# Optimization experiments

Measured on AMD Instinct MI355X. Metric: run time of the kernel, lower is better.

Reference implementation:

```python
import jax, jax.numpy as jnp
import numpy as np

EMBED_DIM = 512
NUM_HEADS = 8
HEAD_DIM = EMBED_DIM // NUM_HEADS


def setup_inputs() -> dict:
    key = jax.random.key(0)
    ks = jax.random.split(key, 6)
    B, S, E = 2, 4096, EMBED_DIM
    scale = 1.0 / np.sqrt(E)
    return {
        "rotation_params": jax.random.normal(ks[0], (E, E), jnp.float32) * scale,
        "entangle_params": jax.random.normal(ks[1], (E, E), jnp.float32) * scale,
        "inputs": jax.random.normal(ks[2], (B, S, E), jnp.float32),
        "w_q": jax.random.normal(ks[3], (E, E), jnp.float32) * scale,
        "w_k": jax.random.normal(ks[4], (E, E), jnp.float32) * scale,
        "w_v": jax.random.normal(ks[5], (E, E), jnp.float32) * scale,
    }


def reference(rotation_params, entangle_params, inputs, w_q, w_k, w_v):
    B, S, E = inputs.shape
    H, D = NUM_HEADS, HEAD_DIM
    # torch nn.Linear(x) = x @ W.T ; then extra matmul with rotation/entangle mats
    q = (inputs @ w_q.T) @ rotation_params  # [B,S,E]
    k = (inputs @ w_k.T) @ entangle_params  # [B,S,E]
    v = inputs @ w_v.T                       # [B,S,E]
    # split heads -> [B,H,S,D]
    q = q.reshape(B, S, H, D).transpose(0, 2, 1, 3)
    k = k.reshape(B, S, H, D).transpose(0, 2, 1, 3)
    v = v.reshape(B, S, H, D).transpose(0, 2, 1, 3)
    scores = jnp.einsum("bhqd,bhkd->bhqk", q, k) / jnp.sqrt(jnp.float32(D))
    attn = jax.nn.softmax(scores, axis=-1)  # dropout p=0 (eval) -> identity
    out = jnp.einsum("bhqk,bhkd->bhqd", attn, v)
    return out.transpose(0, 2, 1, 3).reshape(B, S, E)
```

## Files before the change

### kernel.cpp

```cpp
#include <hip/hip_runtime.h>
#include <cstddef>

#define E 512
#define H 8
#define D 64
#define BATCH 2
#define SEQ 4096

typedef __attribute__((ext_vector_type(8))) short bf16x8;
typedef __attribute__((ext_vector_type(4))) float f32x4;
typedef __attribute__((ext_vector_type(16))) float f32x16;
typedef __attribute__((ext_vector_type(4))) unsigned uint4v;

__device__ __forceinline__ ushort f2bf(float f) {
  unsigned u = __builtin_bit_cast(unsigned, f);
  u += 0x7fff + ((u >> 16) & 1);
  return (ushort)(u >> 16);
}
__device__ __forceinline__ float bf2f(ushort h) {
  return __builtin_bit_cast(float, (unsigned)h << 16);
}
__device__ __forceinline__ unsigned pk_bf16(float lo, float hi) {
#if __has_builtin(__builtin_amdgcn_cvt_pk_bf16_f32)
  typedef __attribute__((ext_vector_type(2))) __bf16 bfv2;
  bfv2 r = __builtin_amdgcn_cvt_pk_bf16_f32(lo, hi);
  return __builtin_bit_cast(unsigned, r);
#else
  return (unsigned)f2bf(lo) | ((unsigned)f2bf(hi) << 16);
#endif
}
__device__ __forceinline__ float fexp2(float x) {
#if __has_builtin(__builtin_amdgcn_exp2f)
  return __builtin_amdgcn_exp2f(x);
#else
  return exp2f(x);
#endif
}
__device__ __forceinline__ void permswap32(unsigned& a, unsigned& b) {
  asm("v_permlane32_swap_b32 %0, %1" : "+v"(a), "+v"(b));
}

__global__ __launch_bounds__(256) void xcast(const float* __restrict__ x,
                                             ushort* __restrict__ xh,
                                             ushort* __restrict__ xl) {
  size_t i = ((size_t)blockIdx.x * 256 + threadIdx.x) * 4;
  float4 v = *(const float4*)&x[i];
  ushort4 h, l;
  h.x = f2bf(v.x); l.x = f2bf(v.x - bf2f(h.x));
  h.y = f2bf(v.y); l.y = f2bf(v.y - bf2f(h.y));
  h.z = f2bf(v.z); l.z = f2bf(v.z - bf2f(h.z));
  h.w = f2bf(v.w); l.w = f2bf(v.w - bf2f(h.w));
  *(ushort4*)&xh[i] = h;
  *(ushort4*)&xl[i] = l;
}

__global__ __launch_bounds__(256) void fold_tiled(
    const float* __restrict__ wq, const float* __restrict__ wk,
    const float* __restrict__ rot, const float* __restrict__ ent,
    ushort* __restrict__ weffbT) {
  const int which = blockIdx.z;
  const float* w = which ? wk : wq;
  const float* r = which ? ent : rot;
  const int k = blockIdx.x * 256 + threadIdx.x;
  const int n0 = blockIdx.y * 8;
  float acc[8] = {};
  for (int j0 = 0; j0 < E; j0 += 16) {
    float wv_[16];
#pragma unroll
    for (int u = 0; u < 16; ++u) wv_[u] = w[(size_t)(j0 + u) * E + k];
#pragma unroll
    for (int u = 0; u < 16; ++u)
#pragma unroll
      for (int t = 0; t < 8; ++t)
        acc[t] += wv_[u] * r[(size_t)(j0 + u) * E + n0 + t];
  }
#pragma unroll
  for (int t = 0; t < 8; ++t)
    weffbT[(size_t)which * E * E + (size_t)(n0 + t) * E + k] = f2bf(acc[t]);
}

__global__ __launch_bounds__(256) void wv_cast(const float* __restrict__ wv,
                                               ushort* __restrict__ dst) {
  size_t i = ((size_t)blockIdx.x * 256 + threadIdx.x) * 4;
  float4 v = *(const float4*)&wv[i];
  ushort4 o;
  o.x = f2bf(v.x); o.y = f2bf(v.y); o.z = f2bf(v.z); o.w = f2bf(v.w);
  *(ushort4*)&dst[i] = o;
}

#define LDQ 72
#define LDS_S 136

__global__ __launch_bounds__(512, 4) void qkv_fused(
    const ushort* __restrict__ xhg, const ushort* __restrict__ xlg,
    const ushort* __restrict__ weffbT, ushort* __restrict__ qg,
    ushort* __restrict__ kg, ushort* __restrict__ vtg) {
  __shared__ ushort sm[(128 + 128 + 192) * LDQ];
  ushort* Ah = sm;
  ushort* Al = sm + 128 * LDQ;
  ushort* Bs = sm + 256 * LDQ;
  ushort* vt_lds = Bs;

  const int lin = blockIdx.y * 8 + blockIdx.x;
  const int nl = (lin & 7) * 64 + (lin >> 3);
  const int head = nl & 7;
  const int m0 = (nl >> 3) * 128;

  const int tid = threadIdx.x;
  const int wave = tid >> 6, lane = tid & 63;
  const int l31 = lane & 31, hi = lane >> 5;
  const int wm = wave & 3, wn = wave >> 2;

  const int ar = tid >> 2, ac8 = (tid & 3) * 8;
  const int b1r = tid >> 2;
  const int b2r = 128 + ((tid >> 2) & 63);

  const ushort* arow = xhg + (size_t)(m0 + ar) * E + ac8;
  const ushort* lrow = xlg + (size_t)(m0 + ar) * E + ac8;
  const ushort* b1row =
      weffbT + (size_t)(b1r >> 6) * E * E + (size_t)(head * 64 + (b1r & 63)) * E + ac8;
  const ushort* b2row =
      weffbT + (size_t)2 * E * E + (size_t)(head * 64 + (b2r & 63)) * E + ac8;

  f32x16 acc[3];
  acc[0] = 0.f;
  acc[1] = 0.f;
  acc[2] = 0.f;

  uint4 pa_h = *(const uint4*)&arow[0];
  uint4 pa_l = *(const uint4*)&lrow[0];
  uint4 pb1 = *(const uint4*)&b1row[0];
  uint4 pb2 = (tid < 256) ? *(const uint4*)&b2row[0] : uint4{0, 0, 0, 0};

  const ushort* Ar = Ah + (wm * 32 + l31) * LDQ;
  const ushort* Lr = Al + (wm * 32 + l31) * LDQ;
  const ushort* Br = Bs + (wn * 96 + l31) * LDQ;

  for (int k0 = 0; k0 < E; k0 += 32) {
    __syncthreads();
    *(uint4*)&Ah[ar * LDQ + ac8] = pa_h;
    *(uint4*)&Al[ar * LDQ + ac8] = pa_l;
    *(uint4*)&Bs[b1r * LDQ + ac8] = pb1;
    if (tid < 256) *(uint4*)&Bs[b2r * LDQ + ac8] = pb2;
    __syncthreads();

    const int kn = (k0 + 32 < E) ? k0 + 32 : 0;
    pa_h = *(const uint4*)&arow[kn];
    pa_l = *(const uint4*)&lrow[kn];
    pb1 = *(const uint4*)&b1row[kn];
    if (tid < 256) pb2 = *(const uint4*)&b2row[kn];

#pragma unroll
    for (int ks = 0; ks < 2; ++ks) {
      bf16x8 ah = *(const bf16x8*)&Ar[ks * 16 + hi * 8];
      bf16x8 al = *(const bf16x8*)&Lr[ks * 16 + hi * 8];
#pragma unroll
      for (int t = 0; t < 3; ++t) {
        bf16x8 bf = *(const bf16x8*)&Br[t * 32 * LDQ + ks * 16 + hi * 8];
        acc[t] =
            __builtin_amdgcn_mfma_f32_32x32x16_bf16(ah, bf, acc[t], 0, 0, 0);
        acc[t] =
            __builtin_amdgcn_mfma_f32_32x32x16_bf16(al, bf, acc[t], 0, 0, 0);
      }
    }
  }

  const int b = m0 >> 12;
  const int s_base = m0 & (SEQ - 1);
  const float QSCALE = 0.125f * 1.44269504f;

#pragma unroll
  for (int t = 0; t < 3; ++t) {
    const int n0 = wn * 96 + t * 32;
    const int w = n0 >> 6;
    if (w != 2) {
      ushort* dst = (w == 0) ? qg : kg;
      const float sc = (w == 0) ? QSCALE : 1.0f;
      const int d = (n0 & 63) + l31;
#pragma unroll
      for (int r = 0; r < 16; ++r) {
        float v = acc[t][r] * sc;
        float vo = __shfl_xor(v, 1);
        if (!(lane & 1)) {
          int s = s_base + wm * 32 + (r & 3) + 8 * (r >> 2) + 4 * hi;
          size_t ix = ((size_t)(b * H + head) * SEQ + s) * D + d;
          *(unsigned*)&dst[ix] = pk_bf16(v, vo);
        }
      }
    }
  }

  __syncthreads();
  if (wn == 1) {
#pragma unroll
    for (int t = 1; t < 3; ++t) {
      const int d = (t - 1) * 32 + l31;
#pragma unroll
      for (int g = 0; g < 4; ++g) {
        uint2 w2;
        w2.x = pk_bf16(acc[t][g * 4 + 0], acc[t][g * 4 + 1]);
        w2.y = pk_bf16(acc[t][g * 4 + 2], acc[t][g * 4 + 3]);
        int s = wm * 32 + 8 * g + 4 * hi;
        *(uint2*)&vt_lds[d * LDS_S + s] = w2;
      }
    }
  }
  __syncthreads();
  {
    int vr = tid >> 3, vs = (tid & 7) * 16;
    uint4 c0 = *(const uint4*)&vt_lds[vr * LDS_S + vs];
    uint4 c1 = *(const uint4*)&vt_lds[vr * LDS_S + vs + 8];
    size_t vo = ((size_t)(b * H + head) * D + vr) * SEQ + s_base + vs;
    *(uint4*)&vtg[vo] = c0;
    *(uint4*)&vtg[vo + 8] = c1;
  }
}

#define LDK 72

__global__ __launch_bounds__(512, 4) void attn_mfma(
    const ushort* __restrict__ qg, const ushort* __restrict__ kg,
    const ushort* __restrict__ vtg, float* __restrict__ out) {
  __shared__ ushort sm[4 * 64 * LDK + 256];
  ushort* Ks0 = sm;
  ushort* Vs0 = sm + 2 * 64 * LDK;
  float* lex = (float*)(sm + 4 * 64 * LDK);

  const int lin = blockIdx.y * gridDim.x + blockIdx.x;
  const int nl = (lin & 7) * 64 + (lin >> 3);
  const int qt = nl & 31;
  const int bh = nl >> 5;

  const int tid = threadIdx.x;
  const int wave = tid >> 6;
  const int grp = wave >> 2, wq = wave & 3;
  const int lane = tid & 63;
  const int l31 = lane & 31, hi = lane >> 5;
  const int gtid = tid & 255;

  const ushort* qp = qg + (size_t)bh * SEQ * D;
  const ushort* kp = kg + (size_t)bh * SEQ * D;
  const ushort* vp = vtg + (size_t)bh * D * SEQ;
  ushort* Ksg = Ks0 + grp * 64 * LDK;
  ushort* Vsg = Vs0 + grp * 64 * LDK;

  const int qrow0 = qt * 128 + wq * 32;
  bf16x8 qf[4];
#pragma unroll
  for (int ds = 0; ds < 4; ++ds)
    qf[ds] =
        *(const bf16x8*)&qp[(size_t)(qrow0 + l31) * D + ds * 16 + hi * 8];

  f32x16 o[2];
  o[0] = 0.f;
  o[1] = 0.f;
  float l_r = 0.f;

  const int r0 = gtid >> 3, c0 = (gtid & 7) * 8;
  const int r1 = 32 + r0;

  uint4 pk0 = *(const uint4*)&kp[(size_t)(grp * 64 + r0) * D + c0];
  uint4 pk1 = *(const uint4*)&kp[(size_t)(grp * 64 + r1) * D + c0];
  uint4 pv0 = *(const uint4*)&vp[(size_t)r0 * SEQ + grp * 64 + c0];
  uint4 pv1 = *(const uint4*)&vp[(size_t)r1 * SEQ + grp * 64 + c0];

  for (int it = 0; it < SEQ / 128; ++it) {
    __syncthreads();
    *(uint4*)&Ksg[r0 * LDK + c0] = pk0;
    *(uint4*)&Ksg[r1 * LDK + c0] = pk1;
    *(uint4*)&Vsg[r0 * LDK + c0] = pv0;
    *(uint4*)&Vsg[r1 * LDK + c0] = pv1;
    __syncthreads();

    {
      const int itn = (it + 1 < SEQ / 128) ? it + 1 : it;
      const int ktn = itn * 2 + grp;
      const ushort* ksrc = kp + (size_t)ktn * 64 * D;
      pk0 = *(const uint4*)&ksrc[r0 * D + c0];
      pk1 = *(const uint4*)&ksrc[r1 * D + c0];
      pv0 = *(const uint4*)&vp[(size_t)r0 * SEQ + ktn * 64 + c0];
      pv1 = *(const uint4*)&vp[(size_t)r1 * SEQ + ktn * 64 + c0];
    }

    __builtin_amdgcn_s_setprio(1);
    f32x16 st0 = 0.f, st1 = 0.f;
#pragma unroll
    for (int ds = 0; ds < 4; ++ds) {
      bf16x8 kf0 = *(const bf16x8*)&Ksg[(l31)*LDK + ds * 16 + hi * 8];
      bf16x8 kf1 = *(const bf16x8*)&Ksg[(32 + l31) * LDK + ds * 16 + hi * 8];
      st0 = __builtin_amdgcn_mfma_f32_32x32x16_bf16(kf0, qf[ds], st0, 0, 0, 0);
      st1 = __builtin_amdgcn_mfma_f32_32x32x16_bf16(kf1, qf[ds], st1, 0, 0, 0);
    }

    bf16x8 pf00, pf01;
    {
      float pv[16];
#pragma unroll
      for (int r = 0; r < 16; ++r) pv[r] = fexp2(st0[r]);
      float s01 = (pv[0] + pv[1]) + (pv[2] + pv[3]);
      float s23 = (pv[4] + pv[5]) + (pv[6] + pv[7]);
      float s45 = (pv[8] + pv[9]) + (pv[10] + pv[11]);
      float s67 = (pv[12] + pv[13]) + (pv[14] + pv[15]);
      l_r += (s01 + s23) + (s45 + s67);
      unsigned w0[4], w1[4];
#pragma unroll
      for (int j = 0; j < 2; ++j) {
        {
          unsigned c0w = pk_bf16(pv[2 * j + 0], pv[2 * j + 1]);
          unsigned c1w = pk_bf16(pv[2 * j + 4], pv[2 * j + 5]);
          permswap32(c0w, c1w);
          w0[j] = c0w;
          w0[2 + j] = c1w;
        }
        {
          unsigned c0w = pk_bf16(pv[2 * j + 8], pv[2 * j + 9]);
          unsigned c1w = pk_bf16(pv[2 * j + 12], pv[2 * j + 13]);
          permswap32(c0w, c1w);
          w1[j] = c0w;
          w1[2 + j] = c1w;
        }
      }
      pf00 = __builtin_bit_cast(bf16x8, (uint4v){w0[0], w0[1], w0[2], w0[3]});
      pf01 = __builtin_bit_cast(bf16x8, (uint4v){w1[0], w1[1], w1[2], w1[3]});
    }
#pragma unroll
    for (int nt = 0; nt < 2; ++nt) {
      bf16x8 vf0 = *(const bf16x8*)&Vsg[(nt * 32 + l31) * LDK + hi * 8];
      o[nt] =
          __builtin_amdgcn_mfma_f32_32x32x16_bf16(pf00, vf0, o[nt], 0, 0, 0);
      bf16x8 vf1 = *(const bf16x8*)&Vsg[(nt * 32 + l31) * LDK + 16 + hi * 8];
      o[nt] =
          __builtin_amdgcn_mfma_f32_32x32x16_bf16(pf01, vf1, o[nt], 0, 0, 0);
    }

    bf16x8 pf10, pf11;
    {
      float pv[16];
#pragma unroll
      for (int r = 0; r < 16; ++r) pv[r] = fexp2(st1[r]);
      float s01 = (pv[0] + pv[1]) + (pv[2] + pv[3]);
      float s23 = (pv[4] + pv[5]) + (pv[6] + pv[7]);
      float s45 = (pv[8] + pv[9]) + (pv[10] + pv[11]);
      float s67 = (pv[12] + pv[13]) + (pv[14] + pv[15]);
      l_r += (s01 + s23) + (s45 + s67);
      unsigned w0[4], w1[4];
#pragma unroll
      for (int j = 0; j < 2; ++j) {
        {
          unsigned c0w = pk_bf16(pv[2 * j + 0], pv[2 * j + 1]);
          unsigned c1w = pk_bf16(pv[2 * j + 4], pv[2 * j + 5]);
          permswap32(c0w, c1w);
          w0[j] = c0w;
          w0[2 + j] = c1w;
        }
        {
          unsigned c0w = pk_bf16(pv[2 * j + 8], pv[2 * j + 9]);
          unsigned c1w = pk_bf16(pv[2 * j + 12], pv[2 * j + 13]);
          permswap32(c0w, c1w);
          w1[j] = c0w;
          w1[2 + j] = c1w;
        }
      }
      pf10 = __builtin_bit_cast(bf16x8, (uint4v){w0[0], w0[1], w0[2], w0[3]});
      pf11 = __builtin_bit_cast(bf16x8, (uint4v){w1[0], w1[1], w1[2], w1[3]});
    }
#pragma unroll
    for (int nt = 0; nt < 2; ++nt) {
      bf16x8 vf0 = *(const bf16x8*)&Vsg[(nt * 32 + l31) * LDK + 32 + hi * 8];
      o[nt] =
          __builtin_amdgcn_mfma_f32_32x32x16_bf16(pf10, vf0, o[nt], 0, 0, 0);
      bf16x8 vf1 = *(const bf16x8*)&Vsg[(nt * 32 + l31) * LDK + 48 + hi * 8];
      o[nt] =
          __builtin_amdgcn_mfma_f32_32x32x16_bf16(pf11, vf1, o[nt], 0, 0, 0);
    }
    __builtin_amdgcn_s_setprio(0);
  }

  __syncthreads();
  float lg = l_r + __shfl_xor(l_r, 32);
  float* Oex = (float*)sm;
  if (grp == 1) {
#pragma unroll
    for (int nt = 0; nt < 2; ++nt)
#pragma unroll
      for (int r = 0; r < 16; ++r) {
        int row = (r & 3) + 8 * (r >> 2) + 4 * hi;
        Oex[(wq * 32 + row) * 68 + nt * 32 + l31] = o[nt][r];
      }
    if (lane < 32) lex[wq * 32 + l31] = lg;
  }
  __syncthreads();
  if (grp == 0) {
    float linv = 1.f / (lg + lex[wq * 32 + l31]);
    const int b = bh >> 3, h = bh & 7;
#pragma unroll
    for (int r = 0; r < 16; ++r) {
      int row = (r & 3) + 8 * (r >> 2) + 4 * hi;
      float inv = __shfl(linv, row);
      int srow = qt * 128 + wq * 32 + row;
#pragma unroll
      for (int nt = 0; nt < 2; ++nt) {
        float val = o[nt][r] + Oex[(wq * 32 + row) * 68 + nt * 32 + l31];
        out[((size_t)b * SEQ + srow) * E + h * D + nt * 32 + l31] = val * inv;
      }
    }
  }
}

extern "C" void kernel_launch(void* const* d_in, const int* in_sizes, int n_in,
                              void* d_out, int out_size, void* d_ws,
                              size_t ws_size, hipStream_t stream) {
  const float* rot = (const float*)d_in[0];
  const float* ent = (const float*)d_in[1];
  const float* x = (const float*)d_in[2];
  const float* wq = (const float*)d_in[3];
  const float* wk = (const float*)d_in[4];
  const float* wv = (const float*)d_in[5];
  float* out = (float*)d_out;

  const size_t NX = (size_t)BATCH * SEQ * E;
  ushort* weffbT = (ushort*)d_ws;
  ushort* xh = weffbT + 3 * E * E;
  ushort* xl = xh + NX;
  ushort* qg = xl + NX;
  ushort* kg = qg + NX;
  ushort* vtg = kg + NX;

  xcast<<<dim3(NX / 1024), 256, 0, stream>>>(x, xh, xl);
  fold_tiled<<<dim3(E / 256, E / 8, 2), 256, 0, stream>>>(wq, wk, rot, ent,
                                                          weffbT);
  wv_cast<<<dim3(E * E / 1024), 256, 0, stream>>>(wv, weffbT + 2 * E * E);
  qkv_fused<<<dim3(H, BATCH * SEQ / 128), 512, 0, stream>>>(xh, xl, weffbT, qg,
                                                            kg, vtg);
  attn_mfma<<<dim3(SEQ / 128, BATCH * H), 512, 0, stream>>>(qg, kg, vtg, out);
}
```

Measured before the change: 232.9 us.

## Merge wv cast into fold kernel, deepen QKV prefetch, simplify attention block mapping

Folds the wv bf16 cast into fold_tiled as a third z-slice, which removes one kernel launch, and halves the per-thread output columns so the fold grid has more blocks. The QKV GEMM loop now keeps two register stages of global prefetch (A/B) and is unrolled by two, giving loads more time to complete before they are stored to LDS. The attention kernel drops its swizzled block-index remapping and uses blockIdx directly, which changes the L2 locality pattern across heads. These are several unrelated tweaks, and the extra prefetch registers in qkv_fused could hurt occupancy.

Result: no change. 231.2 us (-0.7%).

```diff
diff --git a/kernel.cpp b/kernel.cpp
--- a/kernel.cpp
+++ b/kernel.cpp
@@ -57,13 +57,20 @@
 __global__ __launch_bounds__(256) void fold_tiled(
     const float* __restrict__ wq, const float* __restrict__ wk,
     const float* __restrict__ rot, const float* __restrict__ ent,
-    ushort* __restrict__ weffbT) {
-  const int which = blockIdx.z;
-  const float* w = which ? wk : wq;
-  const float* r = which ? ent : rot;
+    const float* __restrict__ wv, ushort* __restrict__ weffbT) {
+  const int z = blockIdx.z;
   const int k = blockIdx.x * 256 + threadIdx.x;
-  const int n0 = blockIdx.y * 8;
-  float acc[8] = {};
+  const int n0 = blockIdx.y * 4;
+  if (z == 2) {
+#pragma unroll
+    for (int t = 0; t < 4; ++t)
+      weffbT[(size_t)2 * E * E + (size_t)(n0 + t) * E + k] =
+          f2bf(wv[(size_t)(n0 + t) * E + k]);
+    return;
+  }
+  const float* w = z ? wk : wq;
+  const float* r = z ? ent : rot;
+  float acc[4] = {};
   for (int j0 = 0; j0 < E; j0 += 16) {
     float wv_[16];
 #pragma unroll
@@ -71,21 +78,12 @@
 #pragma unroll
     for (int u = 0; u < 16; ++u)
 #pragma unroll
-      for (int t = 0; t < 8; ++t)
+      for (int t = 0; t < 4; ++t)
         acc[t] += wv_[u] * r[(size_t)(j0 + u) * E + n0 + t];
   }
 #pragma unroll
-  for (int t = 0; t < 8; ++t)
-    weffbT[(size_t)which * E * E + (size_t)(n0 + t) * E + k] = f2bf(acc[t]);
-}
-
-__global__ __launch_bounds__(256) void wv_cast(const float* __restrict__ wv,
-                                               ushort* __restrict__ dst) {
-  size_t i = ((size_t)blockIdx.x * 256 + threadIdx.x) * 4;
-  float4 v = *(const float4*)&wv[i];
-  ushort4 o;
-  o.x = f2bf(v.x); o.y = f2bf(v.y); o.z = f2bf(v.z); o.w = f2bf(v.w);
-  *(ushort4*)&dst[i] = o;
+  for (int t = 0; t < 4; ++t)
+    weffbT[(size_t)z * E * E + (size_t)(n0 + t) * E + k] = f2bf(acc[t]);
 }
 
 #define LDQ 72
@@ -127,29 +125,11 @@
   acc[1] = 0.f;
   acc[2] = 0.f;
 
-  uint4 pa_h = *(const uint4*)&arow[0];
-  uint4 pa_l = *(const uint4*)&lrow[0];
-  uint4 pb1 = *(const uint4*)&b1row[0];
-  uint4 pb2 = (tid < 256) ? *(const uint4*)&b2row[0] : uint4{0, 0, 0, 0};
-
   const ushort* Ar = Ah + (wm * 32 + l31) * LDQ;
   const ushort* Lr = Al + (wm * 32 + l31) * LDQ;
   const ushort* Br = Bs + (wn * 96 + l31) * LDQ;
 
-  for (int k0 = 0; k0 < E; k0 += 32) {
-    __syncthreads();
-    *(uint4*)&Ah[ar * LDQ + ac8] = pa_h;
-    *(uint4*)&Al[ar * LDQ + ac8] = pa_l;
-    *(uint4*)&Bs[b1r * LDQ + ac8] = pb1;
-    if (tid < 256) *(uint4*)&Bs[b2r * LDQ + ac8] = pb2;
-    __syncthreads();
-
-    const int kn = (k0 + 32 < E) ? k0 + 32 : 0;
-    pa_h = *(const uint4*)&arow[kn];
-    pa_l = *(const uint4*)&lrow[kn];
-    pb1 = *(const uint4*)&b1row[kn];
-    if (tid < 256) pb2 = *(const uint4*)&b2row[kn];
-
+  auto compute = [&]() {
 #pragma unroll
     for (int ks = 0; ks < 2; ++ks) {
       bf16x8 ah = *(const bf16x8*)&Ar[ks * 16 + hi * 8];
@@ -163,6 +143,47 @@
             __builtin_amdgcn_mfma_f32_32x32x16_bf16(al, bf, acc[t], 0, 0, 0);
       }
     }
+  };
+
+  uint4 pa_hA = *(const uint4*)&arow[0];
+  uint4 pa_lA = *(const uint4*)&lrow[0];
+  uint4 pb1A = *(const uint4*)&b1row[0];
+  uint4 pb2A = (tid < 256) ? *(const uint4*)&b2row[0] : uint4{0, 0, 0, 0};
+  uint4 pa_hB = *(const uint4*)&arow[32];
+  uint4 pa_lB = *(const uint4*)&lrow[32];
+  uint4 pb1B = *(const uint4*)&b1row[32];
+  uint4 pb2B = (tid < 256) ? *(const uint4*)&b2row[32] : uint4{0, 0, 0, 0};
+
+  for (int k0 = 0; k0 < E; k0 += 64) {
+    __syncthreads();
+    *(uint4*)&Ah[ar * LDQ + ac8] = pa_hA;
+    *(uint4*)&Al[ar * LDQ + ac8] = pa_lA;
+    *(uint4*)&Bs[b1r * LDQ + ac8] = pb1A;
+    if (tid < 256) *(uint4*)&Bs[b2r * LDQ + ac8] = pb2A;
+    __syncthreads();
+    {
+      const int kA = (k0 + 64 < E) ? k0 + 64 : 0;
+      pa_hA = *(const uint4*)&arow[kA];
+      pa_lA = *(const uint4*)&lrow[kA];
+      pb1A = *(const uint4*)&b1row[kA];
+      if (tid < 256) pb2A = *(const uint4*)&b2row[kA];
+    }
+    compute();
+
+    __syncthreads();
+    *(uint4*)&Ah[ar * LDQ + ac8] = pa_hB;
+    *(uint4*)&Al[ar * LDQ + ac8] = pa_lB;
+    *(uint4*)&Bs[b1r * LDQ + ac8] = pb1B;
+    if (tid < 256) *(uint4*)&Bs[b2r * LDQ + ac8] = pb2B;
+    __syncthreads();
+    {
+      const int kB = (k0 + 96 < E) ? k0 + 96 : 32;
+      pa_hB = *(const uint4*)&arow[kB];
+      pa_lB = *(const uint4*)&lrow[kB];
+      pb1B = *(const uint4*)&b1row[kB];
+      if (tid < 256) pb2B = *(const uint4*)&b2row[kB];
+    }
+    compute();
   }
 
   const int b = m0 >> 12;
@@ -226,11 +247,8 @@
   ushort* Vs0 = sm + 2 * 64 * LDK;
   float* lex = (float*)(sm + 4 * 64 * LDK);
 
-  const int lin = blockIdx.y * gridDim.x + blockIdx.x;
-  const int nl = (lin & 7) * 64 + (lin >> 3);
-  const int qt = nl & 31;
-  const int bh = nl >> 5;
-
+  const int qt = blockIdx.x;
+  const int bh = blockIdx.y;
   const int tid = threadIdx.x;
   const int wave = tid >> 6;
   const int grp = wave >> 2, wq = wave & 3;
@@ -427,9 +445,8 @@
   ushort* vtg = kg + NX;
 
   xcast<<<dim3(NX / 1024), 256, 0, stream>>>(x, xh, xl);
-  fold_tiled<<<dim3(E / 256, E / 8, 2), 256, 0, stream>>>(wq, wk, rot, ent,
+  fold_tiled<<<dim3(E / 256, E / 4, 3), 256, 0, stream>>>(wq, wk, rot, ent, wv,
                                                           weffbT);
-  wv_cast<<<dim3(E * E / 1024), 256, 0, stream>>>(wv, weffbT + 2 * E * E);
   qkv_fused<<<dim3(H, BATCH * SEQ / 128), 512, 0, stream>>>(xh, xl, weffbT, qg,
                                                             kg, vtg);
   attn_mfma<<<dim3(SEQ / 128, BATCH * H), 512, 0, stream>>>(qg, kg, vtg, out);
```
